# Kernel tuning notes

Measured on AMD Instinct MI355X. Metric: run time of the kernel, lower is better.

The kernel has to match this reference:

```python
import jax, jax.numpy as jnp
import numpy as np

B, T, C, E = 16, 392, 512, 512
E8 = E // 8          # dim_project output
K = T // 2           # top_k / number of sampled positions
RECEPTIVE_FIELD = 2.0


def setup_inputs() -> dict:
    key = jax.random.key(0)
    ks = jax.random.split(key, 6)
    s = 0.03  # trunc_normal std used by the module init
    return {
        "x_in": jax.random.normal(ks[0], (B, T, C), jnp.float32),
        "W_dim": jax.random.normal(ks[1], (E8, E), jnp.float32) * s,
        "b_dim": jnp.zeros((E8,), jnp.float32),
        "W_time": jax.random.normal(ks[2], (T, T * T), jnp.float32) * s,
        "b_time": jnp.zeros((T,), jnp.float32),
        "W_offa": jax.random.normal(ks[3], (K, T), jnp.float32) * s,
        "W_offd": jax.random.normal(ks[4], (K, T), jnp.float32) * s,
    }


def _grid_sample_1d(x, idx_norm):
    """Bilinear 1D sample along last axis of x (b,T,c) at normalized coords
    idx_norm (b,K); padding_mode='border', align_corners=False.
    Equivalent to the module's F.grid_sample on (b,T,c,1) with grid (0, g)."""
    c = x.shape[-1]
    ix = ((idx_norm + 1.0) * c - 1.0) * 0.5          # unnormalize (align_corners=False)
    x0 = jnp.floor(ix)
    w1 = ix - x0                                     # fractional weight
    x0i = jnp.clip(x0.astype(jnp.int32), 0, c - 1)   # border clamp
    x1i = jnp.clip(x0.astype(jnp.int32) + 1, 0, c - 1)
    v0 = jnp.take_along_axis(x, x0i[:, None, :], axis=2)  # (b,T,K)
    v1 = jnp.take_along_axis(x, x1i[:, None, :], axis=2)
    return v0 * (1.0 - w1)[:, None, :] + v1 * w1[:, None, :]


def reference(x_in, W_dim, b_dim, W_time, b_time, W_offa, W_offd):
    b, t, c = x_in.shape
    scaler = 1.0 / E
    # dot-similarity attention map
    xi = jnp.einsum('btc,ec->bte', x_in, W_dim) + b_dim          # (b,t,E8)
    att = jax.nn.softmax(scaler * jnp.einsum('bie,bje->bij', xi, xi), axis=-1)
    # giant time projection: (b, t*t) @ (t*t, t)
    xt = att.reshape(b, t * t) @ W_time.T + b_time               # (b,t)
    off_a = jnp.tanh(xt @ W_offa.T) * RECEPTIVE_FIELD            # (b,K)
    off_d = jnp.tanh(xt @ W_offd.T) * RECEPTIVE_FIELD
    idx_a = jnp.arange(0, t, 2, dtype=jnp.float32)[None, :] + off_a
    idx_d = jnp.arange(1, t + 1, 2, dtype=jnp.float32)[None, :] + off_d
    # normalize_grid: n = K*2 = t
    denom = float(max(t - 1, 1))
    g_a = 2.0 * idx_a / denom - 1.0
    g_d = 2.0 * idx_d / denom - 1.0
    x_a = _grid_sample_1d(x_in, g_a)                             # (b,t,K)
    x_d = _grid_sample_1d(x_in, g_d)
    return (x_a, x_d)
```

## Files before the change

kernel.cpp:

```cpp
#include <hip/hip_runtime.h>
#include <hip/hip_bf16.h>

constexpr int BB   = 16;
constexpr int TT_  = 392;
constexpr int CC   = 512;
constexpr int E8_  = 64;
constexpr int KK   = 196;
constexpr long TT2 = 153664;
constexpr long OUT_HALF = 1229312;

constexpr int NC2   = 98;
constexpr int CH2   = 1568;
constexpr int BK2   = 224;
constexpr int NSTEP = 7;
constexpr int LDW   = 232;
constexpr int NJT   = 13;
constexpr int PJ    = 448;

typedef __bf16 bf16_t;
typedef bf16_t bf16x8 __attribute__((ext_vector_type(8)));
typedef float  f32x4  __attribute__((ext_vector_type(4)));

static __device__ __forceinline__ unsigned int pk2(float a, float b) {
    unsigned short lo = __builtin_bit_cast(unsigned short, (bf16_t)a);
    unsigned short hi = __builtin_bit_cast(unsigned short, (bf16_t)b);
    return ((unsigned int)hi << 16) | (unsigned int)lo;
}
static __device__ __forceinline__ float bf2f(unsigned short u) {
    unsigned int w = ((unsigned int)u) << 16;
    return __builtin_bit_cast(float, w);
}

__global__ __launch_bounds__(256) void k_xi(const float* __restrict__ x,
                                            const float* __restrict__ Wd,
                                            const float* __restrict__ bd,
                                            float* __restrict__ xi) {
    __shared__ bf16_t Xl[64 * 40];
    __shared__ bf16_t Wl[64 * 40];
    int m0 = blockIdx.x * 64;
    int tid = threadIdx.x;
    int wv = tid >> 6, lane = tid & 63;
    int n = lane & 15, quad = lane >> 4;
    f32x4 acc[4] = {};
    for (int kt = 0; kt < 16; ++kt) {
        __syncthreads();
        #pragma unroll
        for (int t = 0; t < 2; ++t) {
            int s = t * 256 + tid;
            int r = s >> 3, c4 = s & 7;
            f32x4 xv = *(const f32x4*)(x + (size_t)(m0 + r) * CC + kt * 32 + c4 * 4);
            f32x4 wvv = *(const f32x4*)(Wd + (size_t)r * CC + kt * 32 + c4 * 4);
            *(uint2*)(&Xl[r * 40 + c4 * 4]) = make_uint2(pk2(xv.x, xv.y), pk2(xv.z, xv.w));
            *(uint2*)(&Wl[r * 40 + c4 * 4]) = make_uint2(pk2(wvv.x, wvv.y), pk2(wvv.z, wvv.w));
        }
        __syncthreads();
        bf16x8 a = *(const bf16x8*)(&Xl[(wv * 16 + n) * 40 + quad * 8]);
        #pragma unroll
        for (int nt = 0; nt < 4; ++nt) {
            bf16x8 b = *(const bf16x8*)(&Wl[(nt * 16 + n) * 40 + quad * 8]);
            acc[nt] = __builtin_amdgcn_mfma_f32_16x16x32_bf16(a, b, acc[nt], 0, 0, 0);
        }
    }
    #pragma unroll
    for (int nt = 0; nt < 4; ++nt)
        #pragma unroll
        for (int r = 0; r < 4; ++r) {
            int m = m0 + wv * 16 + quad * 4 + r;
            int e = nt * 16 + n;
            xi[(size_t)m * E8_ + e] = acc[nt][r] + bd[e];
        }
}

__global__ __launch_bounds__(256) void k_att(const float* __restrict__ xi,
                                             unsigned short* __restrict__ att_b) {
    __shared__ bf16_t Xb[400 * 40];
    int b = blockIdx.x, tb = blockIdx.y;
    int tid = threadIdx.x;
    int wv = tid >> 6, lane = tid & 63;
    int n = lane & 15, quad = lane >> 4;
    #pragma unroll
    for (int t = 0; t < 25; ++t) {
        int s = t * 256 + tid;
        int r = s >> 4, c4 = s & 15;
        uint2 v = make_uint2(0u, 0u);
        if (r < TT_) {
            f32x4 xv = *(const f32x4*)(xi + (size_t)(b * TT_ + r) * E8_ + c4 * 4);
            v = make_uint2(pk2(xv.x, xv.y), pk2(xv.z, xv.w));
        }
        *(uint2*)(&Xb[r * 40 + c4 * 4]) = v;
    }
    __syncthreads();
    int arow = tb * 64 + wv * 16 + n;
    if (arow > 399) arow = 399;
    bf16x8 a0 = *(const bf16x8*)(&Xb[arow * 40]);
    bf16x8 a1 = *(const bf16x8*)(&Xb[arow * 40 + 32]);
    f32x4 acc[25];
    #pragma unroll
    for (int nt = 0; nt < 25; ++nt) acc[nt] = (f32x4){0.f, 0.f, 0.f, 0.f};
    #pragma unroll
    for (int nt = 0; nt < 25; ++nt) {
        bf16x8 b0 = *(const bf16x8*)(&Xb[(nt * 16 + n) * 40]);
        bf16x8 b1 = *(const bf16x8*)(&Xb[(nt * 16 + n) * 40 + 32]);
        acc[nt] = __builtin_amdgcn_mfma_f32_16x16x32_bf16(a0, b0, acc[nt], 0, 0, 0);
        acc[nt] = __builtin_amdgcn_mfma_f32_16x16x32_bf16(a1, b1, acc[nt], 0, 0, 0);
    }
    const float scaler = 1.0f / 512.0f;
    float mx[4] = {-1e30f, -1e30f, -1e30f, -1e30f};
    #pragma unroll
    for (int nt = 0; nt < 25; ++nt) {
        bool valid = (nt * 16 + n) < TT_;
        #pragma unroll
        for (int r = 0; r < 4; ++r) {
            float v = valid ? acc[nt][r] * scaler : -1e30f;
            acc[nt][r] = v;
            mx[r] = fmaxf(mx[r], v);
        }
    }
    #pragma unroll
    for (int r = 0; r < 4; ++r) {
        #pragma unroll
        for (int o = 1; o < 16; o <<= 1) mx[r] = fmaxf(mx[r], __shfl_xor(mx[r], o, 64));
    }
    float sm[4] = {0.f, 0.f, 0.f, 0.f};
    #pragma unroll
    for (int nt = 0; nt < 25; ++nt)
        #pragma unroll
        for (int r = 0; r < 4; ++r) {
            float e = __expf(acc[nt][r] - mx[r]);
            acc[nt][r] = e;
            sm[r] += e;
        }
    #pragma unroll
    for (int r = 0; r < 4; ++r) {
        #pragma unroll
        for (int o = 1; o < 16; o <<= 1) sm[r] += __shfl_xor(sm[r], o, 64);
        sm[r] = 1.0f / sm[r];
    }
    unsigned short* dst = att_b + (size_t)b * TT2;
    #pragma unroll
    for (int r = 0; r < 4; ++r) {
        int ti = tb * 64 + wv * 16 + quad * 4 + r;
        if (ti < TT_) {
            #pragma unroll
            for (int nt = 0; nt < 25; ++nt) {
                int tj = nt * 16 + n;
                if (tj < TT_)
                    dst[(size_t)ti * TT_ + tj] =
                        __builtin_bit_cast(unsigned short, (bf16_t)(acc[nt][r] * sm[r]));
            }
        }
    }
}

__global__ __launch_bounds__(128) void k_xt(const float* __restrict__ Wt,
                                            const unsigned short* __restrict__ att_b,
                                            unsigned short* __restrict__ part_b) {
    __shared__ bf16_t Wl[32 * LDW];
    __shared__ bf16_t Al[16 * LDW];
    int c = blockIdx.x, jt = blockIdx.y;
    int tid = threadIdx.x;
    int wv = tid >> 6, lane = tid & 63;
    int n = lane & 15, quad = lane >> 4;
    f32x4 acc = {0.f, 0.f, 0.f, 0.f};
    long kbase = (long)c * CH2;
    for (int s = 0; s < NSTEP; ++s) {
        long k0 = kbase + (long)s * BK2;
        __syncthreads();
        #pragma unroll
        for (int t = 0; t < 14; ++t) {
            int idx = t * 128 + tid;
            int r = idx / 56, col = idx - r * 56;
            int jg = jt * 32 + r; if (jg > 391) jg = 391;
            f32x4 w = *(const f32x4*)(Wt + (size_t)jg * TT2 + k0 + col * 4);
            *(uint2*)(&Wl[r * LDW + col * 4]) = make_uint2(pk2(w.x, w.y), pk2(w.z, w.w));
        }
        #pragma unroll
        for (int t = 0; t < 4; ++t) {
            int idx = t * 128 + tid;
            if (idx < 448) {
                int r = idx / 28, q = idx - r * 28;
                uint4 v = *(const uint4*)(att_b + (size_t)r * TT2 + k0 + q * 8);
                *(uint4*)(&Al[r * LDW + q * 8]) = v;
            }
        }
        __syncthreads();
        #pragma unroll
        for (int m = 0; m < 7; ++m) {
            int k = m * 32;
            bf16x8 a = *(const bf16x8*)(&Al[n * LDW + k + quad * 8]);
            bf16x8 b = *(const bf16x8*)(&Wl[(wv * 16 + n) * LDW + k + quad * 8]);
            acc = __builtin_amdgcn_mfma_f32_16x16x32_bf16(a, b, acc, 0, 0, 0);
        }
    }
    int j = jt * 32 + wv * 16 + n;
    #pragma unroll
    for (int r = 0; r < 4; ++r) {
        int m = quad * 4 + r;
        part_b[(size_t)c * (16 * PJ) + (size_t)m * PJ + j] =
            __builtin_bit_cast(unsigned short, (bf16_t)acc[r]);
    }
}

__global__ __launch_bounds__(256) void k_reduce_xt(const unsigned short* __restrict__ part_b,
                                                   const float* __restrict__ bt,
                                                   float* __restrict__ xt) {
    int o = blockIdx.x * 256 + threadIdx.x;
    if (o >= 16 * 56) return;
    int b = o / 56, c8 = o - b * 56;
    float s[8] = {};
    for (int c = 0; c < NC2; ++c) {
        uint4 v = *(const uint4*)(part_b + (size_t)c * (16 * PJ) + (size_t)b * PJ + c8 * 8);
        unsigned int w[4] = {v.x, v.y, v.z, v.w};
        #pragma unroll
        for (int t = 0; t < 4; ++t) {
            s[t * 2 + 0] += bf2f((unsigned short)(w[t] & 0xffffu));
            s[t * 2 + 1] += bf2f((unsigned short)(w[t] >> 16));
        }
    }
    #pragma unroll
    for (int t = 0; t < 8; ++t) {
        int j = c8 * 8 + t;
        if (j < TT_) xt[(size_t)b * TT_ + j] = s[t] + bt[j];
    }
}

__global__ __launch_bounds__(256) void k_off(const float* __restrict__ xt,
                                             const float* __restrict__ Wa,
                                             const float* __restrict__ Wd,
                                             float* __restrict__ wix) {
    int o = blockIdx.x * 256 + threadIdx.x;
    if (o >= 2 * BB * KK) return;
    int which = o / (BB * KK);
    int rem = o - which * (BB * KK);
    int b = rem / KK;
    int k = rem - b * KK;
    const f32x4* __restrict__ wr = (const f32x4*)((which ? Wd : Wa) + (size_t)k * TT_);
    const f32x4* __restrict__ xr = (const f32x4*)(xt + (size_t)b * TT_);
    float acc = 0.f;
    #pragma unroll 2
    for (int q = 0; q < TT_ / 4; ++q) {
        f32x4 w = wr[q], x = xr[q];
        acc += w.x * x.x + w.y * x.y + w.z * x.z + w.w * x.w;
    }
    float off = tanhf(acc) * 2.0f;
    float idx = (float)(2 * k + which) + off;
    float g = 2.0f * idx / 391.0f - 1.0f;
    float ix = ((g + 1.0f) * 512.0f - 1.0f) * 0.5f;
    wix[o] = ix;
}

__global__ __launch_bounds__(256) void k_sample(const float* __restrict__ x,
                                                const float* __restrict__ wix,
                                                float* __restrict__ out) {
    __shared__ float xr[4][512];
    int b = blockIdx.x, t0 = blockIdx.y * 4;
    int tid = threadIdx.x;
    const float* src = x + ((size_t)b * TT_ + t0) * CC;
    #pragma unroll
    for (int s = 0; s < 8; ++s) {
        int idx = s * 256 + tid;
        ((float*)xr)[idx] = src[idx];
    }
    __syncthreads();
    for (int w = tid; w < 2 * 4 * KK; w += 256) {
        int which = (w >= 4 * KK) ? 1 : 0;
        int rem = w - which * 4 * KK;
        int tl = rem / KK;
        int k = rem - tl * KK;
        float ix = wix[(size_t)which * (BB * KK) + b * KK + k];
        float x0f = floorf(ix);
        float w1 = ix - x0f;
        int c0 = (int)x0f;
        int c1 = c0 + 1;
        c0 = min(max(c0, 0), CC - 1);
        c1 = min(max(c1, 0), CC - 1);
        float v0 = xr[tl][c0], v1 = xr[tl][c1];
        out[(size_t)which * OUT_HALF + ((size_t)(b * TT_) + t0 + tl) * KK + k] =
            v0 * (1.0f - w1) + v1 * w1;
    }
}

extern "C" void kernel_launch(void* const* d_in, const int* in_sizes, int n_in,
                              void* d_out, int out_size, void* d_ws, size_t ws_size,
                              hipStream_t stream) {
    const float* x_in   = (const float*)d_in[0];
    const float* W_dim  = (const float*)d_in[1];
    const float* b_dim  = (const float*)d_in[2];
    const float* W_time = (const float*)d_in[3];
    const float* b_time = (const float*)d_in[4];
    const float* W_offa = (const float*)d_in[5];
    const float* W_offd = (const float*)d_in[6];
    float* out = (float*)d_out;
    float* ws  = (float*)d_ws;

    unsigned short* att_b  = (unsigned short*)ws;
    float*          xi     = ws + 1229312;
    unsigned short* part_b = (unsigned short*)(ws + 1630720);
    float*          xt     = ws + 1981952;
    float*          wix    = ws + 1988224;

    k_xi<<<98, 256, 0, stream>>>(x_in, W_dim, b_dim, xi);
    k_att<<<dim3(BB, 7), 256, 0, stream>>>(xi, att_b);
    k_xt<<<dim3(NC2, NJT), 128, 0, stream>>>(W_time, att_b, part_b);
    k_reduce_xt<<<4, 256, 0, stream>>>(part_b, b_time, xt);
    k_off<<<25, 256, 0, stream>>>(xt, W_offa, W_offd, wix);
    k_sample<<<dim3(BB, TT_ / 4), 256, 0, stream>>>(x_in, wix, out);
}
```

Baseline: 441.8 us.

## Replace split-K partials and reduce kernel with atomics, repad LDS, vectorize sampling loads

The k_reduce_xt kernel is dropped: k_xt now accumulates its split-K partials straight into xt with float atomics, and k_xi zeroes xt first. The b_time bias is folded into k_off's dot product. LDS row strides change (232→228, 40→36/68) and fragment loads are split into two 8-byte reads to avoid bank conflicts. k_sample now copies the x rows with 16-byte vector loads. Atomics add contention and make the summation order nondeterministic. The old reduction summed bf16-rounded partials, while the new path accumulates in fp32.

```diff
diff --git a/kernel.cpp b/kernel.cpp
--- a/kernel.cpp
+++ b/kernel.cpp
@@ -13,9 +13,10 @@
 constexpr int CH2   = 1568;
 constexpr int BK2   = 224;
 constexpr int NSTEP = 7;
-constexpr int LDW   = 232;
 constexpr int NJT   = 13;
-constexpr int PJ    = 448;
+constexpr int LDW = 228;
+constexpr int LDX = 36;
+constexpr int LDA = 68;
 
 typedef __bf16 bf16_t;
 typedef bf16_t bf16x8 __attribute__((ext_vector_type(8)));
@@ -26,19 +27,26 @@
     unsigned short hi = __builtin_bit_cast(unsigned short, (bf16_t)b);
     return ((unsigned int)hi << 16) | (unsigned int)lo;
 }
-static __device__ __forceinline__ float bf2f(unsigned short u) {
-    unsigned int w = ((unsigned int)u) << 16;
-    return __builtin_bit_cast(float, w);
+static __device__ __forceinline__ bf16x8 ld_frag(const bf16_t* p) {
+    uint2 lo = *(const uint2*)p;
+    uint2 hi = *(const uint2*)(p + 4);
+    uint4 u = make_uint4(lo.x, lo.y, hi.x, hi.y);
+    return __builtin_bit_cast(bf16x8, u);
 }
 
 __global__ __launch_bounds__(256) void k_xi(const float* __restrict__ x,
                                             const float* __restrict__ Wd,
                                             const float* __restrict__ bd,
-                                            float* __restrict__ xi) {
-    __shared__ bf16_t Xl[64 * 40];
-    __shared__ bf16_t Wl[64 * 40];
+                                            float* __restrict__ xi,
+                                            float* __restrict__ xt) {
+    __shared__ bf16_t Xl[64 * LDX];
+    __shared__ bf16_t Wl[64 * LDX];
+    int tid = threadIdx.x;
+    if (blockIdx.x < 25) {
+        int o = blockIdx.x * 256 + tid;
+        if (o < BB * TT_) xt[o] = 0.f;
+    }
     int m0 = blockIdx.x * 64;
-    int tid = threadIdx.x;
     int wv = tid >> 6, lane = tid & 63;
     int n = lane & 15, quad = lane >> 4;
     f32x4 acc[4] = {};
@@ -49,15 +57,15 @@
             int s = t * 256 + tid;
             int r = s >> 3, c4 = s & 7;
             f32x4 xv = *(const f32x4*)(x + (size_t)(m0 + r) * CC + kt * 32 + c4 * 4);
-            f32x4 wvv = *(const f32x4*)(Wd + (size_t)r * CC + kt * 32 + c4 * 4);
-            *(uint2*)(&Xl[r * 40 + c4 * 4]) = make_uint2(pk2(xv.x, xv.y), pk2(xv.z, xv.w));
-            *(uint2*)(&Wl[r * 40 + c4 * 4]) = make_uint2(pk2(wvv.x, wvv.y), pk2(wvv.z, wvv.w));
-        }
-        __syncthreads();
-        bf16x8 a = *(const bf16x8*)(&Xl[(wv * 16 + n) * 40 + quad * 8]);
+            f32x4 wq = *(const f32x4*)(Wd + (size_t)r * CC + kt * 32 + c4 * 4);
+            *(uint2*)(&Xl[r * LDX + c4 * 4]) = make_uint2(pk2(xv.x, xv.y), pk2(xv.z, xv.w));
+            *(uint2*)(&Wl[r * LDX + c4 * 4]) = make_uint2(pk2(wq.x, wq.y), pk2(wq.z, wq.w));
+        }
+        __syncthreads();
+        bf16x8 a = ld_frag(&Xl[(wv * 16 + n) * LDX + quad * 8]);
         #pragma unroll
         for (int nt = 0; nt < 4; ++nt) {
-            bf16x8 b = *(const bf16x8*)(&Wl[(nt * 16 + n) * 40 + quad * 8]);
+            bf16x8 b = ld_frag(&Wl[(nt * 16 + n) * LDX + quad * 8]);
             acc[nt] = __builtin_amdgcn_mfma_f32_16x16x32_bf16(a, b, acc[nt], 0, 0, 0);
         }
     }
@@ -73,7 +81,7 @@
 
 __global__ __launch_bounds__(256) void k_att(const float* __restrict__ xi,
                                              unsigned short* __restrict__ att_b) {
-    __shared__ bf16_t Xb[400 * 40];
+    __shared__ bf16_t Xb[400 * LDA];
     int b = blockIdx.x, tb = blockIdx.y;
     int tid = threadIdx.x;
     int wv = tid >> 6, lane = tid & 63;
@@ -87,20 +95,20 @@
             f32x4 xv = *(const f32x4*)(xi + (size_t)(b * TT_ + r) * E8_ + c4 * 4);
             v = make_uint2(pk2(xv.x, xv.y), pk2(xv.z, xv.w));
         }
-        *(uint2*)(&Xb[r * 40 + c4 * 4]) = v;
+        *(uint2*)(&Xb[r * LDA + c4 * 4]) = v;
     }
     __syncthreads();
     int arow = tb * 64 + wv * 16 + n;
     if (arow > 399) arow = 399;
-    bf16x8 a0 = *(const bf16x8*)(&Xb[arow * 40]);
-    bf16x8 a1 = *(const bf16x8*)(&Xb[arow * 40 + 32]);
+    bf16x8 a0 = ld_frag(&Xb[arow * LDA + quad * 8]);
+    bf16x8 a1 = ld_frag(&Xb[arow * LDA + 32 + quad * 8]);
     f32x4 acc[25];
     #pragma unroll
     for (int nt = 0; nt < 25; ++nt) acc[nt] = (f32x4){0.f, 0.f, 0.f, 0.f};
     #pragma unroll
     for (int nt = 0; nt < 25; ++nt) {
-        bf16x8 b0 = *(const bf16x8*)(&Xb[(nt * 16 + n) * 40]);
-        bf16x8 b1 = *(const bf16x8*)(&Xb[(nt * 16 + n) * 40 + 32]);
+        bf16x8 b0 = ld_frag(&Xb[(nt * 16 + n) * LDA + quad * 8]);
+        bf16x8 b1 = ld_frag(&Xb[(nt * 16 + n) * LDA + 32 + quad * 8]);
         acc[nt] = __builtin_amdgcn_mfma_f32_16x16x32_bf16(a0, b0, acc[nt], 0, 0, 0);
         acc[nt] = __builtin_amdgcn_mfma_f32_16x16x32_bf16(a1, b1, acc[nt], 0, 0, 0);
     }
@@ -154,7 +162,7 @@
 
 __global__ __launch_bounds__(128) void k_xt(const float* __restrict__ Wt,
                                             const unsigned short* __restrict__ att_b,
-                                            unsigned short* __restrict__ part_b) {
+                                            float* __restrict__ xt) {
     __shared__ bf16_t Wl[32 * LDW];
     __shared__ bf16_t Al[16 * LDW];
     int c = blockIdx.x, jt = blockIdx.y;
@@ -180,51 +188,31 @@
             if (idx < 448) {
                 int r = idx / 28, q = idx - r * 28;
                 uint4 v = *(const uint4*)(att_b + (size_t)r * TT2 + k0 + q * 8);
-                *(uint4*)(&Al[r * LDW + q * 8]) = v;
+                *(uint2*)(&Al[r * LDW + q * 8])     = make_uint2(v.x, v.y);
+                *(uint2*)(&Al[r * LDW + q * 8 + 4]) = make_uint2(v.z, v.w);
             }
         }
         __syncthreads();
         #pragma unroll
         for (int m = 0; m < 7; ++m) {
             int k = m * 32;
-            bf16x8 a = *(const bf16x8*)(&Al[n * LDW + k + quad * 8]);
-            bf16x8 b = *(const bf16x8*)(&Wl[(wv * 16 + n) * LDW + k + quad * 8]);
+            bf16x8 a = ld_frag(&Al[n * LDW + k + quad * 8]);
+            bf16x8 b = ld_frag(&Wl[(wv * 16 + n) * LDW + k + quad * 8]);
             acc = __builtin_amdgcn_mfma_f32_16x16x32_bf16(a, b, acc, 0, 0, 0);
         }
     }
     int j = jt * 32 + wv * 16 + n;
-    #pragma unroll
-    for (int r = 0; r < 4; ++r) {
-        int m = quad * 4 + r;
-        part_b[(size_t)c * (16 * PJ) + (size_t)m * PJ + j] =
-            __builtin_bit_cast(unsigned short, (bf16_t)acc[r]);
-    }
-}
-
-__global__ __launch_bounds__(256) void k_reduce_xt(const unsigned short* __restrict__ part_b,
-                                                   const float* __restrict__ bt,
-                                                   float* __restrict__ xt) {
-    int o = blockIdx.x * 256 + threadIdx.x;
-    if (o >= 16 * 56) return;
-    int b = o / 56, c8 = o - b * 56;
-    float s[8] = {};
-    for (int c = 0; c < NC2; ++c) {
-        uint4 v = *(const uint4*)(part_b + (size_t)c * (16 * PJ) + (size_t)b * PJ + c8 * 8);
-        unsigned int w[4] = {v.x, v.y, v.z, v.w};
-        #pragma unroll
-        for (int t = 0; t < 4; ++t) {
-            s[t * 2 + 0] += bf2f((unsigned short)(w[t] & 0xffffu));
-            s[t * 2 + 1] += bf2f((unsigned short)(w[t] >> 16));
-        }
-    }
-    #pragma unroll
-    for (int t = 0; t < 8; ++t) {
-        int j = c8 * 8 + t;
-        if (j < TT_) xt[(size_t)b * TT_ + j] = s[t] + bt[j];
+    if (j < TT_) {
+        #pragma unroll
+        for (int r = 0; r < 4; ++r) {
+            int m = quad * 4 + r;
+            unsafeAtomicAdd(&xt[(size_t)m * TT_ + j], acc[r]);
+        }
     }
 }
 
 __global__ __launch_bounds__(256) void k_off(const float* __restrict__ xt,
+                                             const float* __restrict__ bt,
                                              const float* __restrict__ Wa,
                                              const float* __restrict__ Wd,
                                              float* __restrict__ wix) {
@@ -236,11 +224,13 @@
     int k = rem - b * KK;
     const f32x4* __restrict__ wr = (const f32x4*)((which ? Wd : Wa) + (size_t)k * TT_);
     const f32x4* __restrict__ xr = (const f32x4*)(xt + (size_t)b * TT_);
+    const f32x4* __restrict__ br = (const f32x4*)bt;
     float acc = 0.f;
     #pragma unroll 2
     for (int q = 0; q < TT_ / 4; ++q) {
-        f32x4 w = wr[q], x = xr[q];
-        acc += w.x * x.x + w.y * x.y + w.z * x.z + w.w * x.w;
+        f32x4 w = wr[q], x = xr[q], bb = br[q];
+        acc += (x.x + bb.x) * w.x + (x.y + bb.y) * w.y
+             + (x.z + bb.z) * w.z + (x.w + bb.w) * w.w;
     }
     float off = tanhf(acc) * 2.0f;
     float idx = (float)(2 * k + which) + off;
@@ -257,9 +247,9 @@
     int tid = threadIdx.x;
     const float* src = x + ((size_t)b * TT_ + t0) * CC;
     #pragma unroll
-    for (int s = 0; s < 8; ++s) {
+    for (int s = 0; s < 2; ++s) {
         int idx = s * 256 + tid;
-        ((float*)xr)[idx] = src[idx];
+        ((f32x4*)xr)[idx] = ((const f32x4*)src)[idx];
     }
     __syncthreads();
     for (int w = tid; w < 2 * 4 * KK; w += 256) {
@@ -293,16 +283,14 @@
     float* out = (float*)d_out;
     float* ws  = (float*)d_ws;
 
-    unsigned short* att_b  = (unsigned short*)ws;
-    float*          xi     = ws + 1229312;
-    unsigned short* part_b = (unsigned short*)(ws + 1630720);
-    float*          xt     = ws + 1981952;
-    float*          wix    = ws + 1988224;
-
-    k_xi<<<98, 256, 0, stream>>>(x_in, W_dim, b_dim, xi);
+    unsigned short* att_b = (unsigned short*)ws;
+    float*          xi    = ws + 1229312;
+    float*          xt    = ws + 1630720;
+    float*          wix   = ws + 1636992;
+
+    k_xi<<<98, 256, 0, stream>>>(x_in, W_dim, b_dim, xi, xt);
     k_att<<<dim3(BB, 7), 256, 0, stream>>>(xi, att_b);
-    k_xt<<<dim3(NC2, NJT), 128, 0, stream>>>(W_time, att_b, part_b);
-    k_reduce_xt<<<4, 256, 0, stream>>>(part_b, b_time, xt);
-    k_off<<<25, 256, 0, stream>>>(xt, W_offa, W_offd, wix);
+    k_xt<<<dim3(NC2, NJT), 128, 0, stream>>>(W_time, att_b, xt);
+    k_off<<<25, 256, 0, stream>>>(xt, b_time, W_offa, W_offd, wix);
     k_sample<<<dim3(BB, TT_ / 4), 256, 0, stream>>>(x_in, wix, out);
 }
```

New measurement: 407.0 us. -7.9%, faster.
